# Performance work log

Hardware: AMD Instinct MI355X
Metric: run time of the kernel (lower is better)

## Reference

```python
import jax, jax.numpy as jnp
import numpy as np

B, C, K, H, W = 2, 8, 2048, 128, 128


def setup_inputs() -> dict:
    key = jax.random.key(0)
    k1, k2, k3 = jax.random.split(key, 3)
    image_real = jax.random.normal(k1, (B, C, H, W), dtype=jnp.float32)
    image_imag = jax.random.normal(k2, (B, C, H, W), dtype=jnp.float32)
    # k-space trajectory in radians/voxel, convention of torchkbnufft: [-pi, pi]
    kspace_traj = jax.random.uniform(
        k3, (B, C, 2, K), dtype=jnp.float32, minval=-np.pi, maxval=np.pi
    )
    return {"image_real": image_real, "image_imag": image_imag, "kspace_traj": kspace_traj}


def reference(image_real, image_imag, kspace_traj):
    """Exact type-2 non-uniform DFT (the math that the Kaiser-Bessel NUFFT
    in generate_nufft_op approximates), double-vmapped over (batch, coil).

    out[b,c,k] = sum_{x,y} image[b,c,x,y] * exp(-i*(om_x[b,c,k]*gx[x] + om_y[b,c,k]*gy[y]))
    with a centered image grid gx = x - H//2, gy = y - W//2.
    The kernel is separable in x/y, so we contract in two einsums instead of
    materializing a (B,C,K,H*W) phase matrix.
    """
    image = image_real + 1j * image_imag  # (B,C,H,W) complex64
    h, w = image.shape[-2:]
    gx = (jnp.arange(h) - h // 2).astype(jnp.float32)  # centered grid coords
    gy = (jnp.arange(w) - w // 2).astype(jnp.float32)

    om_x = kspace_traj[..., 0, :]  # (B,C,K)
    om_y = kspace_traj[..., 1, :]  # (B,C,K)

    px = jnp.exp(-1j * om_x[..., None] * gx)  # (B,C,K,H)
    py = jnp.exp(-1j * om_y[..., None] * gy)  # (B,C,K,W)

    tmp = jnp.einsum("bcxy,bcky->bckx", image, py)  # contract y first
    out = jnp.einsum("bckx,bckx->bck", tmp, px)  # (B,C,K) complex64
    return out
```

## Files before the change

kernel.cpp:

```cpp
#include <hip/hip_runtime.h>
#include <math.h>


using half8  = __attribute__((ext_vector_type(8))) _Float16;
using f32x4  = __attribute__((ext_vector_type(4))) float;

constexpr int Bn = 2, Cn = 8, Kn = 2048, Hn = 128, Wn = 128;
constexpr int BC  = Bn * Cn;
constexpr int KPW = 16;
constexpr int WPB = 4;
constexpr int KPB = KPW * WPB;
constexpr int NKS = Hn / 32;
constexpr int PSLOTS = 64 * Wn / 8;

__device__ inline void cmul(float& ar, float& ai, float br, float bi) {
    float nr = fmaf(ar, br, -ai * bi);
    ai = fmaf(ar, bi, ai * br);
    ar = nr;
}
__device__ inline void csq(float& r, float& i) {
    float nr = fmaf(r, r, -i * i);
    i = 2.f * r * i;
    r = nr;
}

template<int OUT_COMPLEX>
__global__ __launch_bounds__(256, 4)
void nufft_mfma(const float* __restrict__ img_re, const float* __restrict__ img_im,
                const float* __restrict__ traj, float* __restrict__ out)
{
    __shared__ half8 re_lds[PSLOTS];
    __shared__ half8 im_lds[PSLOTS];

    const int bc   = blockIdx.x / (Kn / KPB);
    const int kt   = blockIdx.x % (Kn / KPB);
    const int wave = threadIdx.x >> 6;
    const int lane = threadIdx.x & 63;
    const int xlo  = lane & 15;
    const int grp  = lane >> 4;
    const int kbase = kt * KPB + wave * KPW;
    const size_t ibase = (size_t)bc * Hn * Wn;

    auto STAGE = [&](int p) {
        #pragma unroll
        for (int i = 0; i < 4; ++i) {
            const int s = i * 256 + (int)threadIdx.x;
            const int xl = s >> 4;
            const int j = (s & 15) ^ (xl & 7);
            const float* gr = img_re + ibase + (size_t)(p * 64 + xl) * Wn + j * 8;
            const float* gi = img_im + ibase + (size_t)(p * 64 + xl) * Wn + j * 8;
            float4 a = ((const float4*)gr)[0], b = ((const float4*)gr)[1];
            float4 d = ((const float4*)gi)[0], e = ((const float4*)gi)[1];
            half8 hr, hi;
            hr[0]=(_Float16)a.x; hr[1]=(_Float16)a.y; hr[2]=(_Float16)a.z; hr[3]=(_Float16)a.w;
            hr[4]=(_Float16)b.x; hr[5]=(_Float16)b.y; hr[6]=(_Float16)b.z; hr[7]=(_Float16)b.w;
            hi[0]=(_Float16)d.x; hi[1]=(_Float16)d.y; hi[2]=(_Float16)d.z; hi[3]=(_Float16)d.w;
            hi[4]=(_Float16)e.x; hi[5]=(_Float16)e.y; hi[6]=(_Float16)e.z; hi[7]=(_Float16)e.w;
            re_lds[s] = hr;
            im_lds[s] = hi;
        }
    };

    STAGE(0);

    const float om_y = traj[(size_t)(bc * 2 + 1) * Kn + (kbase + xlo)];
    float s, c;
    sincosf(om_y, &s, &c);
    const float syr = c, syi = -s;
    sincosf(om_y * (float)(grp * 8 - 64), &s, &c);
    const float pr0 = c, pi0 = -s;
    float t32r = syr, t32i = syi;
    #pragma unroll
    for (int q = 0; q < 5; ++q) csq(t32r, t32i);

    f32x4 accr[8], acci[8];
    #pragma unroll
    for (int a = 0; a < 8; ++a) { accr[a] = (f32x4)0.f; acci[a] = (f32x4)0.f; }

    __syncthreads();

    #pragma unroll
    for (int p = 0; p < 2; ++p) {
        float pr = pr0, pi = pi0;
        for (int kk = 0; kk < NKS; ++kk) {
            float vr[8], vi[8];
            vr[0] = pr; vi[0] = pi;
            #pragma unroll
            for (int j = 1; j < 8; ++j) {
                float nr = fmaf(vr[j-1], syr, -vi[j-1] * syi);
                vi[j]    = fmaf(vr[j-1], syi,  vi[j-1] * syr);
                vr[j]    = nr;
            }
            half8 ar, ai8, ani;
            #pragma unroll
            for (int j = 0; j < 8; ++j) {
                ar[j]  = (_Float16)vr[j];
                ai8[j] = (_Float16)vi[j];
                ani[j] = (_Float16)(-vi[j]);
            }
            cmul(pr, pi, t32r, t32i);

            const int jx = (kk * 4 + grp) ^ (xlo & 7);
            #pragma unroll
            for (int xt = 0; xt < 4; ++xt) {
                const int slot = (xt * 16 + xlo) * 16 + jx;
                half8 br = re_lds[slot];
                half8 bi = im_lds[slot];
                const int a = p * 4 + xt;
                accr[a] = __builtin_amdgcn_mfma_f32_16x16x32_f16(ar,  br, accr[a], 0, 0, 0);
                accr[a] = __builtin_amdgcn_mfma_f32_16x16x32_f16(ani, bi, accr[a], 0, 0, 0);
                acci[a] = __builtin_amdgcn_mfma_f32_16x16x32_f16(ar,  bi, acci[a], 0, 0, 0);
                acci[a] = __builtin_amdgcn_mfma_f32_16x16x32_f16(ai8, br, acci[a], 0, 0, 0);
            }
        }
        if (p == 0) {
            __syncthreads();
            STAGE(1);
            __syncthreads();
        }
    }

    float outr[4], outi[4];
    #pragma unroll
    for (int r = 0; r < 4; ++r) {
        const int kr = kbase + grp * 4 + r;
        const float om_x = traj[(size_t)(bc * 2 + 0) * Kn + kr];
        sincosf(om_x, &s, &c);
        float t16r = c, t16i = -s;
        sincosf(om_x * (float)(xlo - 64), &s, &c);
        float qr = c, qi = -s;
        #pragma unroll
        for (int q = 0; q < 4; ++q) csq(t16r, t16i);
        float orr = 0.f, oii = 0.f;
        #pragma unroll
        for (int a = 0; a < 8; ++a) {
            const float tre = accr[a][r], tim = acci[a][r];
            orr = fmaf(tre, qr, orr); orr = fmaf(-tim, qi, orr);
            oii = fmaf(tre, qi, oii); oii = fmaf( tim, qr, oii);
            cmul(qr, qi, t16r, t16i);
        }
        #pragma unroll
        for (int m = 1; m < 16; m <<= 1) {
            orr += __shfl_xor(orr, m, 64);
            oii += __shfl_xor(oii, m, 64);
        }
        outr[r] = orr; outi[r] = oii;
    }

    if (xlo == 0) {
        #pragma unroll
        for (int r = 0; r < 4; ++r) {
            const int kr = kbase + grp * 4 + r;
            if (OUT_COMPLEX) {
                out[((size_t)bc * Kn + kr) * 2 + 0] = outr[r];
                out[((size_t)bc * Kn + kr) * 2 + 1] = outi[r];
            } else {
                out[(size_t)bc * Kn + kr] = outr[r];
            }
        }
    }
}

extern "C" void kernel_launch(void* const* d_in, const int* in_sizes, int n_in,
                              void* d_out, int out_size, void* d_ws, size_t ws_size,
                              hipStream_t stream) {
    const float* img_re = (const float*)d_in[0];
    const float* img_im = (const float*)d_in[1];
    const float* traj   = (const float*)d_in[2];
    float* out = (float*)d_out;

    dim3 grid(BC * (Kn / KPB));
    dim3 block(WPB * 64);
    const bool cplx = (out_size == BC * Kn * 2);

    if (cplx) hipLaunchKernelGGL((nufft_mfma<1>), grid, block, 0, stream, img_re, img_im, traj, out);
    else      hipLaunchKernelGGL((nufft_mfma<0>), grid, block, 0, stream, img_re, img_im, traj, out);
}
```

Measured before the change: 12.79 us.

## Double-buffer LDS image tiles and precompute phase fragments to overlap loads with MFMA

Splits image staging into a register load step and an LDS write step, using two LDS buffers so the second half's global loads are in flight during the first half's MFMA compute. This removes one barrier. The y-phase A-fragments for all k-steps are precomputed once and reused across both halves instead of being regenerated per half, and the x-phase twiddles are computed before the main loop. The cost is much higher register and LDS use, so launch bounds drop from 4 to 2 blocks per CU, which lowers occupancy.

```diff
diff --git a/kernel.cpp b/kernel.cpp
--- a/kernel.cpp
+++ b/kernel.cpp
@@ -25,102 +25,90 @@
 }
 
 template<int OUT_COMPLEX>
-__global__ __launch_bounds__(256, 4)
+__global__ __launch_bounds__(256, 2)
 void nufft_mfma(const float* __restrict__ img_re, const float* __restrict__ img_im,
                 const float* __restrict__ traj, float* __restrict__ out)
 {
-    __shared__ half8 re_lds[PSLOTS];
-    __shared__ half8 im_lds[PSLOTS];
+    __shared__ half8 re_lds[2][PSLOTS];
+    __shared__ half8 im_lds[2][PSLOTS];
 
     const int bc   = blockIdx.x / (Kn / KPB);
     const int kt   = blockIdx.x % (Kn / KPB);
+    const int lane = threadIdx.x & 63;
     const int wave = threadIdx.x >> 6;
-    const int lane = threadIdx.x & 63;
     const int xlo  = lane & 15;
     const int grp  = lane >> 4;
     const int kbase = kt * KPB + wave * KPW;
     const size_t ibase = (size_t)bc * Hn * Wn;
 
-    auto STAGE = [&](int p) {
+    float4 sa[4], sb[4], sd[4], se[4];
+
+    int s_idx[4], s_j[4], s_xl[4];
+    #pragma unroll
+    for (int i = 0; i < 4; ++i) {
+        const int s = i * 256 + (int)threadIdx.x;
+        s_idx[i] = s;
+        s_xl[i]  = s >> 4;
+        s_j[i]   = (s & 15) ^ (s_xl[i] & 7);
+    }
+
+    auto LOADS = [&](int p) {
         #pragma unroll
         for (int i = 0; i < 4; ++i) {
-            const int s = i * 256 + (int)threadIdx.x;
-            const int xl = s >> 4;
-            const int j = (s & 15) ^ (xl & 7);
-            const float* gr = img_re + ibase + (size_t)(p * 64 + xl) * Wn + j * 8;
-            const float* gi = img_im + ibase + (size_t)(p * 64 + xl) * Wn + j * 8;
-            float4 a = ((const float4*)gr)[0], b = ((const float4*)gr)[1];
-            float4 d = ((const float4*)gi)[0], e = ((const float4*)gi)[1];
+            const float* gr = img_re + ibase + (size_t)(p * 64 + s_xl[i]) * Wn + s_j[i] * 8;
+            const float* gi = img_im + ibase + (size_t)(p * 64 + s_xl[i]) * Wn + s_j[i] * 8;
+            sa[i] = ((const float4*)gr)[0];
+            sb[i] = ((const float4*)gr)[1];
+            sd[i] = ((const float4*)gi)[0];
+            se[i] = ((const float4*)gi)[1];
+        }
+    };
+    auto WRITE_LDS = [&](int b) {
+        #pragma unroll
+        for (int i = 0; i < 4; ++i) {
             half8 hr, hi;
-            hr[0]=(_Float16)a.x; hr[1]=(_Float16)a.y; hr[2]=(_Float16)a.z; hr[3]=(_Float16)a.w;
-            hr[4]=(_Float16)b.x; hr[5]=(_Float16)b.y; hr[6]=(_Float16)b.z; hr[7]=(_Float16)b.w;
-            hi[0]=(_Float16)d.x; hi[1]=(_Float16)d.y; hi[2]=(_Float16)d.z; hi[3]=(_Float16)d.w;
-            hi[4]=(_Float16)e.x; hi[5]=(_Float16)e.y; hi[6]=(_Float16)e.z; hi[7]=(_Float16)e.w;
-            re_lds[s] = hr;
-            im_lds[s] = hi;
+            hr[0]=(_Float16)sa[i].x; hr[1]=(_Float16)sa[i].y; hr[2]=(_Float16)sa[i].z; hr[3]=(_Float16)sa[i].w;
+            hr[4]=(_Float16)sb[i].x; hr[5]=(_Float16)sb[i].y; hr[6]=(_Float16)sb[i].z; hr[7]=(_Float16)sb[i].w;
+            hi[0]=(_Float16)sd[i].x; hi[1]=(_Float16)sd[i].y; hi[2]=(_Float16)sd[i].z; hi[3]=(_Float16)sd[i].w;
+            hi[4]=(_Float16)se[i].x; hi[5]=(_Float16)se[i].y; hi[6]=(_Float16)se[i].z; hi[7]=(_Float16)se[i].w;
+            re_lds[b][s_idx[i]] = hr;
+            im_lds[b][s_idx[i]] = hi;
         }
     };
 
-    STAGE(0);
+    LOADS(0);
 
     const float om_y = traj[(size_t)(bc * 2 + 1) * Kn + (kbase + xlo)];
     float s, c;
     sincosf(om_y, &s, &c);
     const float syr = c, syi = -s;
     sincosf(om_y * (float)(grp * 8 - 64), &s, &c);
-    const float pr0 = c, pi0 = -s;
+    float pr = c, pi = -s;
     float t32r = syr, t32i = syi;
     #pragma unroll
     for (int q = 0; q < 5; ++q) csq(t32r, t32i);
 
-    f32x4 accr[8], acci[8];
-    #pragma unroll
-    for (int a = 0; a < 8; ++a) { accr[a] = (f32x4)0.f; acci[a] = (f32x4)0.f; }
-
-    __syncthreads();
-
-    #pragma unroll
-    for (int p = 0; p < 2; ++p) {
-        float pr = pr0, pi = pi0;
-        for (int kk = 0; kk < NKS; ++kk) {
-            float vr[8], vi[8];
-            vr[0] = pr; vi[0] = pi;
-            #pragma unroll
-            for (int j = 1; j < 8; ++j) {
-                float nr = fmaf(vr[j-1], syr, -vi[j-1] * syi);
-                vi[j]    = fmaf(vr[j-1], syi,  vi[j-1] * syr);
-                vr[j]    = nr;
-            }
-            half8 ar, ai8, ani;
-            #pragma unroll
-            for (int j = 0; j < 8; ++j) {
-                ar[j]  = (_Float16)vr[j];
-                ai8[j] = (_Float16)vi[j];
-                ani[j] = (_Float16)(-vi[j]);
-            }
-            cmul(pr, pi, t32r, t32i);
-
-            const int jx = (kk * 4 + grp) ^ (xlo & 7);
-            #pragma unroll
-            for (int xt = 0; xt < 4; ++xt) {
-                const int slot = (xt * 16 + xlo) * 16 + jx;
-                half8 br = re_lds[slot];
-                half8 bi = im_lds[slot];
-                const int a = p * 4 + xt;
-                accr[a] = __builtin_amdgcn_mfma_f32_16x16x32_f16(ar,  br, accr[a], 0, 0, 0);
-                accr[a] = __builtin_amdgcn_mfma_f32_16x16x32_f16(ani, bi, accr[a], 0, 0, 0);
-                acci[a] = __builtin_amdgcn_mfma_f32_16x16x32_f16(ar,  bi, acci[a], 0, 0, 0);
-                acci[a] = __builtin_amdgcn_mfma_f32_16x16x32_f16(ai8, br, acci[a], 0, 0, 0);
-            }
-        }
-        if (p == 0) {
-            __syncthreads();
-            STAGE(1);
-            __syncthreads();
-        }
-    }
-
-    float outr[4], outi[4];
+    half8 Ar[NKS], Ai8[NKS], An[NKS];
+    #pragma unroll
+    for (int kk = 0; kk < NKS; ++kk) {
+        float vr[8], vi[8];
+        vr[0] = pr; vi[0] = pi;
+        #pragma unroll
+        for (int j = 1; j < 8; ++j) {
+            float nr = fmaf(vr[j-1], syr, -vi[j-1] * syi);
+            vi[j]    = fmaf(vr[j-1], syi,  vi[j-1] * syr);
+            vr[j]    = nr;
+        }
+        #pragma unroll
+        for (int j = 0; j < 8; ++j) {
+            Ar[kk][j]  = (_Float16)vr[j];
+            Ai8[kk][j] = (_Float16)vi[j];
+            An[kk][j]  = (_Float16)(-vi[j]);
+        }
+        cmul(pr, pi, t32r, t32i);
+    }
+
+    float eqr[4], eqi[4], etr[4], eti[4];
     #pragma unroll
     for (int r = 0; r < 4; ++r) {
         const int kr = kbase + grp * 4 + r;
@@ -128,9 +116,50 @@
         sincosf(om_x, &s, &c);
         float t16r = c, t16i = -s;
         sincosf(om_x * (float)(xlo - 64), &s, &c);
-        float qr = c, qi = -s;
+        eqr[r] = c; eqi[r] = -s;
         #pragma unroll
         for (int q = 0; q < 4; ++q) csq(t16r, t16i);
+        etr[r] = t16r; eti[r] = t16i;
+    }
+
+    f32x4 accr[8], acci[8];
+    #pragma unroll
+    for (int a = 0; a < 8; ++a) { accr[a] = (f32x4)0.f; acci[a] = (f32x4)0.f; }
+
+    WRITE_LDS(0);
+    __syncthreads();
+
+    LOADS(1);
+
+    auto COMPUTE = [&](int p) {
+        for (int kk = 0; kk < NKS; ++kk) {
+            const int jx = (kk * 4 + grp) ^ (xlo & 7);
+            #pragma unroll
+            for (int xt = 0; xt < 4; ++xt) {
+                const int slot = (xt * 16 + xlo) * 16 + jx;
+                half8 br = re_lds[p][slot];
+                half8 bi = im_lds[p][slot];
+                const int a = p * 4 + xt;
+                accr[a] = __builtin_amdgcn_mfma_f32_16x16x32_f16(Ar[kk], br, accr[a], 0, 0, 0);
+                accr[a] = __builtin_amdgcn_mfma_f32_16x16x32_f16(An[kk], bi, accr[a], 0, 0, 0);
+                acci[a] = __builtin_amdgcn_mfma_f32_16x16x32_f16(Ar[kk], bi, acci[a], 0, 0, 0);
+                acci[a] = __builtin_amdgcn_mfma_f32_16x16x32_f16(Ai8[kk], br, acci[a], 0, 0, 0);
+            }
+        }
+    };
+
+    COMPUTE(0);
+
+    WRITE_LDS(1);
+    __syncthreads();
+
+    COMPUTE(1);
+
+    float outr[4], outi[4];
+    #pragma unroll
+    for (int r = 0; r < 4; ++r) {
+        float qr = eqr[r], qi = eqi[r];
+        const float t16r = etr[r], t16i = eti[r];
         float orr = 0.f, oii = 0.f;
         #pragma unroll
         for (int a = 0; a < 8; ++a) {
```

Result: slower. 13.22 us (+3.3%).
